# Optimization experiments

Measured on AMD Instinct MI355X. Metric: run time of the kernel, lower is better.

Reference implementation:

```python
import math
import jax, jax.numpy as jnp
import numpy as np

Q_MAX = 127.0  # 2**(8-1) - 1 for n_bits=8
SCALE_EPS = 1e-5


def _hadamard_matrix(n):
    H = np.array([[1.0]], dtype=np.float32)
    while H.shape[0] < n:
        H = np.block([[H, H], [H, -H]])
    return jnp.asarray(H)


def quantize_per_channel_absmax(w):
    # per output-channel absmax quantize-dequantize (torch weight per_channel)
    scales = jnp.clip(jnp.max(jnp.abs(w), axis=-1, keepdims=True) / Q_MAX, SCALE_EPS, None)
    return jnp.round(w / scales) * scales


def quantize_per_token_absmax(x):
    # per-token (last-dim) absmax quantize-dequantize
    scales = jnp.clip(jnp.max(jnp.abs(x), axis=-1, keepdims=True) / Q_MAX, SCALE_EPS, None)
    return jnp.round(x / scales) * scales


def setup_inputs() -> dict:
    key = jax.random.key(0)
    k1, k2, k3 = jax.random.split(key, 3)
    B, S, D_IN, D_OUT = 2, 2048, 4096, 4096
    x = jax.random.normal(k1, (B, S, D_IN), dtype=jnp.float32)
    # weight quantized at __init__ time (per_channel, 8-bit), as in the wrapper
    weight = quantize_per_channel_absmax(
        jax.random.normal(k2, (D_OUT, D_IN), dtype=jnp.float32) * (1.0 / math.sqrt(D_IN)))
    bias = jax.random.normal(k3, (D_OUT,), dtype=jnp.float32)
    return {"x": x, "weight": weight, "bias": bias, "had_dim": 64}


def reference(x, weight, bias, had_dim):
    # --- online_partial_had, K == 1 path ---
    B, S, D = x.shape
    n_groups = D // had_dim
    H = _hadamard_matrix(n_groups).astype(x.dtype)
    xr = x.reshape(-1, n_groups, had_dim)  # (B*S, G, had_dim)
    # hadamard_transform along the group axis, scale = 1/sqrt(G)
    xr = jnp.einsum('hg,bgd->bhd', H, xr) * (1.0 / math.sqrt(n_groups))
    x = xr.reshape(B, S, D)
    # --- per-token absmax activation quant ---
    x = quantize_per_token_absmax(x)
    # --- linear with (already quantized) weight ---
    return jnp.einsum('bsd,od->bso', x, weight) + bias
```

## Files before the change

### kernel.cpp

```cpp
#include <hip/hip_runtime.h>

#define M_DIM 4096
#define N_DIM 4096
#define K_DIM 4096

typedef __attribute__((ext_vector_type(4))) int i32x4;
typedef __attribute__((ext_vector_type(16))) int i32x16;

typedef __attribute__((address_space(1))) const void GV;
typedef __attribute__((address_space(3))) void LV;

__global__ __launch_bounds__(256) void prequant_kernel(const float* __restrict__ x,
                                                       const float* __restrict__ w,
                                                       char* __restrict__ xq,
                                                       char* __restrict__ wq,
                                                       float* __restrict__ sx,
                                                       float* __restrict__ sw) {
  const int wave = threadIdx.x >> 6;
  const int lane = threadIdx.x & 63;

  if (blockIdx.x >= 1024) {
    const int row = (blockIdx.x - 1024) * 4 + wave;
    const float* wp = w + (size_t)row * 4096;
    float4 v[16];
#pragma unroll
    for (int c = 0; c < 16; ++c) v[c] = *(const float4*)(wp + c * 256 + lane * 4);
    float amax = 0.f;
#pragma unroll
    for (int c = 0; c < 16; ++c)
      amax = fmaxf(amax, fmaxf(fmaxf(fabsf(v[c].x), fabsf(v[c].y)),
                               fmaxf(fabsf(v[c].z), fabsf(v[c].w))));
#pragma unroll
    for (int off = 32; off >= 1; off >>= 1) amax = fmaxf(amax, __shfl_xor(amax, off, 64));
    amax = fmaxf(amax, 1e-30f);
    const float inv = 127.0f / amax;
    char* op = wq + (size_t)row * 4096;
#pragma unroll
    for (int c = 0; c < 16; ++c) {
      char4 o;
      o.x = (char)rintf(v[c].x * inv);
      o.y = (char)rintf(v[c].y * inv);
      o.z = (char)rintf(v[c].z * inv);
      o.w = (char)rintf(v[c].w * inv);
      *(char4*)(op + c * 256 + lane * 4) = o;
    }
    if (lane == 0) sw[row] = amax * (1.0f / 127.0f);
    return;
  }

  const int tok = blockIdx.x * 4 + wave;
  const int gs = lane >> 4;
  const int q = lane & 15;
  const float* xp = x + (size_t)tok * 4096;

  float4 v[16];
#pragma unroll
  for (int gl = 0; gl < 16; ++gl)
    v[gl] = *(const float4*)(xp + (gl * 4 + gs) * 64 + q * 4);

#pragma unroll
  for (int s = 1; s < 16; s <<= 1) {
#pragma unroll
    for (int i = 0; i < 16; ++i) {
      if ((i & s) == 0) {
        float4 a = v[i], b = v[i | s];
        v[i].x = a.x + b.x; v[i].y = a.y + b.y; v[i].z = a.z + b.z; v[i].w = a.w + b.w;
        v[i | s].x = a.x - b.x; v[i | s].y = a.y - b.y;
        v[i | s].z = a.z - b.z; v[i | s].w = a.w - b.w;
      }
    }
  }
#pragma unroll
  for (int st = 0; st < 2; ++st) {
    const int L = 16 << st;
    const bool hi = (lane & L) != 0;
#pragma unroll
    for (int i = 0; i < 16; ++i) {
      float4 t;
      t.x = __shfl_xor(v[i].x, L, 64);
      t.y = __shfl_xor(v[i].y, L, 64);
      t.z = __shfl_xor(v[i].z, L, 64);
      t.w = __shfl_xor(v[i].w, L, 64);
      if (hi) {
        v[i].x = t.x - v[i].x; v[i].y = t.y - v[i].y;
        v[i].z = t.z - v[i].z; v[i].w = t.w - v[i].w;
      } else {
        v[i].x += t.x; v[i].y += t.y; v[i].z += t.z; v[i].w += t.w;
      }
    }
  }

  float amax = 0.f;
#pragma unroll
  for (int i = 0; i < 16; ++i) {
    v[i].x *= 0.125f; v[i].y *= 0.125f; v[i].z *= 0.125f; v[i].w *= 0.125f;
    amax = fmaxf(amax, fmaxf(fmaxf(fabsf(v[i].x), fabsf(v[i].y)),
                             fmaxf(fabsf(v[i].z), fabsf(v[i].w))));
  }
#pragma unroll
  for (int off = 32; off >= 1; off >>= 1) amax = fmaxf(amax, __shfl_xor(amax, off, 64));

  const float s = fmaxf(amax * (1.0f / 127.0f), 1e-5f);
  const float inv = 1.0f / s;

  char* op = xq + (size_t)tok * 4096;
#pragma unroll
  for (int gl = 0; gl < 16; ++gl) {
    char4 o;
    o.x = (char)rintf(v[gl].x * inv);
    o.y = (char)rintf(v[gl].y * inv);
    o.z = (char)rintf(v[gl].z * inv);
    o.w = (char)rintf(v[gl].w * inv);
    *(char4*)(op + (gl * 4 + gs) * 64 + q * 4) = o;
  }
  if (lane == 0) sx[tok] = s;
}

__global__ __launch_bounds__(256, 2) void gemm_i8(const char* __restrict__ A,
                                                  const char* __restrict__ B,
                                                  const float* __restrict__ sx,
                                                  const float* __restrict__ sw,
                                                  const float* __restrict__ bias,
                                                  float* __restrict__ C) {
  __shared__ __align__(16) char sm[73728];

  const int tid = threadIdx.x;
  const int lane = tid & 63;
  const int wave = tid >> 6;
  const int wm = wave >> 1;
  const int wn = wave & 1;
  const int m32 = lane & 31;
  const int half = lane >> 5;

  const int bid = blockIdx.x;
  const int cx = bid & 7, idx = bid >> 3;
  const int bm = (cx & 3) * 4 + (idx >> 4);
  const int bn = (cx >> 2) * 16 + (idx & 15);

  const int strow = tid >> 2;
  const int sseg = ((tid & 3) ^ ((tid >> 3) & 3)) << 4;
  const char* gA0 = A + (size_t)(bm * 256 + strow) * K_DIM + sseg;
  const char* gB0 = B + (size_t)(bn * 128 + strow) * K_DIM + sseg;

#define STAGE(BUFOFF, KO)                                                                \
  {                                                                                      \
    char* d_ = sm + (BUFOFF) + (tid << 4);                                               \
    __builtin_amdgcn_global_load_lds((GV*)(gA0 + (KO)), (LV*)d_, 16, 0, 0);              \
    __builtin_amdgcn_global_load_lds((GV*)(gA0 + 64 * (size_t)K_DIM + (KO)),             \
                                     (LV*)(d_ + 4096), 16, 0, 0);                        \
    __builtin_amdgcn_global_load_lds((GV*)(gA0 + 128 * (size_t)K_DIM + (KO)),            \
                                     (LV*)(d_ + 8192), 16, 0, 0);                        \
    __builtin_amdgcn_global_load_lds((GV*)(gA0 + 192 * (size_t)K_DIM + (KO)),            \
                                     (LV*)(d_ + 12288), 16, 0, 0);                       \
    __builtin_amdgcn_global_load_lds((GV*)(gB0 + (KO)), (LV*)(d_ + 16384), 16, 0, 0);    \
    __builtin_amdgcn_global_load_lds((GV*)(gB0 + 64 * (size_t)K_DIM + (KO)),             \
                                     (LV*)(d_ + 20480), 16, 0, 0);                       \
  }

  const int aBase = (wm * 128 + m32) * 64;
  const int bBase = 16384 + (wn * 64 + m32) * 64;
  int sl[2];
#pragma unroll
  for (int kc = 0; kc < 2; ++kc) sl[kc] = ((kc * 2 + half) ^ ((m32 >> 1) & 3)) << 4;

  i32x16 acc[4][2];
#pragma unroll
  for (int i = 0; i < 4; ++i)
#pragma unroll
    for (int j = 0; j < 2; ++j)
#pragma unroll
      for (int r = 0; r < 16; ++r) acc[i][j][r] = 0;

  STAGE(0, 0);
  STAGE(24576, 64);
  asm volatile("s_waitcnt vmcnt(6)" ::: "memory");
  __builtin_amdgcn_s_barrier();
  __builtin_amdgcn_sched_barrier(0);

  int o0 = 0, o1 = 24576, o2 = 49152;

#pragma unroll 1
  for (int t = 0; t < 64; ++t) {
    const char* bufp = sm + o0;

    i32x4 af[2][4], bf[2][2];
#pragma unroll
    for (int kc = 0; kc < 2; ++kc) {
#pragma unroll
      for (int fm = 0; fm < 4; ++fm)
        af[kc][fm] = *(const i32x4*)(bufp + aBase + fm * 2048 + sl[kc]);
#pragma unroll
      for (int fn = 0; fn < 2; ++fn)
        bf[kc][fn] = *(const i32x4*)(bufp + bBase + fn * 2048 + sl[kc]);
    }

    if (t < 62) STAGE(o2, (size_t)(t + 2) * 64);

    __builtin_amdgcn_s_setprio(1);
#pragma unroll
    for (int kc = 0; kc < 2; ++kc)
#pragma unroll
      for (int fm = 0; fm < 4; ++fm)
#pragma unroll
        for (int fn = 0; fn < 2; ++fn)
          acc[fm][fn] =
              __builtin_amdgcn_mfma_i32_32x32x32_i8(af[kc][fm], bf[kc][fn], acc[fm][fn], 0, 0, 0);
    __builtin_amdgcn_s_setprio(0);

    if (t < 62) {
      asm volatile("s_waitcnt vmcnt(6)" ::: "memory");
    } else if (t == 62) {
      asm volatile("s_waitcnt vmcnt(0)" ::: "memory");
    }
    if (t < 63) {
      __builtin_amdgcn_s_barrier();
      __builtin_amdgcn_sched_barrier(0);
    }
    const int tmp = o0; o0 = o1; o1 = o2; o2 = tmp;
  }
#undef STAGE

  const int col0 = bn * 128 + wn * 64 + m32;
  const float swv0 = sw[col0];
  const float swv1 = sw[col0 + 32];
  const float bv0 = bias[col0];
  const float bv1 = bias[col0 + 32];

#pragma unroll
  for (int fm = 0; fm < 4; ++fm) {
    const int rbase = bm * 256 + wm * 128 + fm * 32 + 4 * half;
    float sxv[16];
#pragma unroll
    for (int r = 0; r < 16; ++r) sxv[r] = sx[rbase + (r & 3) + 8 * (r >> 2)];
#pragma unroll
    for (int fn = 0; fn < 2; ++fn) {
      const int colg = col0 + fn * 32;
      const float swb = fn ? swv1 : swv0;
      const float bvb = fn ? bv1 : bv0;
#pragma unroll
      for (int r = 0; r < 16; ++r) {
        const int rowg = rbase + (r & 3) + 8 * (r >> 2);
        C[(size_t)rowg * N_DIM + colg] = (float)acc[fm][fn][r] * (sxv[r] * swb) + bvb;
      }
    }
  }
}

extern "C" void kernel_launch(void* const* d_in, const int* in_sizes, int n_in,
                              void* d_out, int out_size, void* d_ws, size_t ws_size,
                              hipStream_t stream) {
  const float* x = (const float*)d_in[0];
  const float* w = (const float*)d_in[1];
  const float* bias = (const float*)d_in[2];

  char* xq = (char*)d_ws;
  char* wq = xq + (size_t)M_DIM * K_DIM;
  float* sx = (float*)(wq + (size_t)N_DIM * K_DIM);
  float* sw = sx + M_DIM;
  float* out = (float*)d_out;

  prequant_kernel<<<2048, 256, 0, stream>>>(x, w, xq, wq, sx, sw);

  gemm_i8<<<dim3(512), dim3(256), 0, stream>>>(xq, wq, sx, sw, bias, out);
}
```

Baseline: 247.7 us.

## Prepack quantized weights in MFMA fragment order and load B directly to registers

The weight prequant pass now writes int8 weights in a pre-swizzled layout matching the MFMA B-fragment order, staging through LDS for coalesced stores. The GEMM no longer stages B tiles in shared memory. Each wave loads its B fragments straight from global memory into registers, double-buffered across even and odd k-steps, and LDS shrinks from 72KB to 48KB. This cuts LDS traffic and B ds_reads, but adds global-load latency exposure and more register pressure.

```diff
diff --git a/kernel.cpp b/kernel.cpp
--- a/kernel.cpp
+++ b/kernel.cpp
@@ -16,6 +16,7 @@
                                                        char* __restrict__ wq,
                                                        float* __restrict__ sx,
                                                        float* __restrict__ sw) {
+  __shared__ char lb[4][4096];
   const int wave = threadIdx.x >> 6;
   const int lane = threadIdx.x & 63;
 
@@ -34,7 +35,6 @@
     for (int off = 32; off >= 1; off >>= 1) amax = fmaxf(amax, __shfl_xor(amax, off, 64));
     amax = fmaxf(amax, 1e-30f);
     const float inv = 127.0f / amax;
-    char* op = wq + (size_t)row * 4096;
 #pragma unroll
     for (int c = 0; c < 16; ++c) {
       char4 o;
@@ -42,7 +42,14 @@
       o.y = (char)rintf(v[c].y * inv);
       o.z = (char)rintf(v[c].z * inv);
       o.w = (char)rintf(v[c].w * inv);
-      *(char4*)(op + c * 256 + lane * 4) = o;
+      *(char4*)(&lb[wave][c * 256 + lane * 4]) = o;
+    }
+    asm volatile("s_waitcnt lgkmcnt(0)" ::: "memory");
+    const size_t pbase = (size_t)(row >> 5) * 131072 + (size_t)(row & 31) * 16;
+#pragma unroll
+    for (int j = 0; j < 4; ++j) {
+      i32x4 ch = *(const i32x4*)(&lb[wave][lane * 64 + j * 16]);
+      *(i32x4*)(wq + pbase + (size_t)(2 * lane + (j >> 1)) * 1024 + (j & 1) * 512) = ch;
     }
     if (lane == 0) sw[row] = amax * (1.0f / 127.0f);
     return;
@@ -122,7 +129,7 @@
                                                   const float* __restrict__ sw,
                                                   const float* __restrict__ bias,
                                                   float* __restrict__ C) {
-  __shared__ __align__(16) char sm[73728];
+  __shared__ __align__(16) char sm[49152];
 
   const int tid = threadIdx.x;
   const int lane = tid & 63;
@@ -140,25 +147,25 @@
   const int strow = tid >> 2;
   const int sseg = ((tid & 3) ^ ((tid >> 3) & 3)) << 4;
   const char* gA0 = A + (size_t)(bm * 256 + strow) * K_DIM + sseg;
-  const char* gB0 = B + (size_t)(bn * 128 + strow) * K_DIM + sseg;
-
-#define STAGE(BUFOFF, KO)                                                                \
-  {                                                                                      \
-    char* d_ = sm + (BUFOFF) + (tid << 4);                                               \
-    __builtin_amdgcn_global_load_lds((GV*)(gA0 + (KO)), (LV*)d_, 16, 0, 0);              \
-    __builtin_amdgcn_global_load_lds((GV*)(gA0 + 64 * (size_t)K_DIM + (KO)),             \
-                                     (LV*)(d_ + 4096), 16, 0, 0);                        \
-    __builtin_amdgcn_global_load_lds((GV*)(gA0 + 128 * (size_t)K_DIM + (KO)),            \
-                                     (LV*)(d_ + 8192), 16, 0, 0);                        \
-    __builtin_amdgcn_global_load_lds((GV*)(gA0 + 192 * (size_t)K_DIM + (KO)),            \
-                                     (LV*)(d_ + 12288), 16, 0, 0);                       \
-    __builtin_amdgcn_global_load_lds((GV*)(gB0 + (KO)), (LV*)(d_ + 16384), 16, 0, 0);    \
-    __builtin_amdgcn_global_load_lds((GV*)(gB0 + 64 * (size_t)K_DIM + (KO)),             \
-                                     (LV*)(d_ + 20480), 16, 0, 0);                       \
-  }
+
+#define STAGE(BUFOFF, KO)                                                              \
+  {                                                                                    \
+    char* d_ = sm + (BUFOFF) + (tid << 4);                                             \
+    __builtin_amdgcn_global_load_lds((GV*)(gA0 + (KO)), (LV*)d_, 16, 0, 0);            \
+    __builtin_amdgcn_global_load_lds((GV*)(gA0 + 64 * (size_t)K_DIM + (KO)),           \
+                                     (LV*)(d_ + 4096), 16, 0, 0);                      \
+    __builtin_amdgcn_global_load_lds((GV*)(gA0 + 128 * (size_t)K_DIM + (KO)),          \
+                                     (LV*)(d_ + 8192), 16, 0, 0);                      \
+    __builtin_amdgcn_global_load_lds((GV*)(gA0 + 192 * (size_t)K_DIM + (KO)),          \
+                                     (LV*)(d_ + 12288), 16, 0, 0);                     \
+  }
+
+  const char* gBf[2];
+#pragma unroll
+  for (int fn = 0; fn < 2; ++fn)
+    gBf[fn] = B + (size_t)(bn * 4 + wn * 2 + fn) * 131072 + (lane << 4);
 
   const int aBase = (wm * 128 + m32) * 64;
-  const int bBase = 16384 + (wn * 64 + m32) * 64;
   int sl[2];
 #pragma unroll
   for (int kc = 0; kc < 2; ++kc) sl[kc] = ((kc * 2 + half) ^ ((m32 >> 1) & 3)) << 4;
@@ -171,53 +178,62 @@
 #pragma unroll
       for (int r = 0; r < 16; ++r) acc[i][j][r] = 0;
 
+  i32x4 bE[2][2], bO[2][2];
+
   STAGE(0, 0);
-  STAGE(24576, 64);
-  asm volatile("s_waitcnt vmcnt(6)" ::: "memory");
+#pragma unroll
+  for (int kc = 0; kc < 2; ++kc)
+#pragma unroll
+    for (int fn = 0; fn < 2; ++fn)
+      bE[kc][fn] = *(const i32x4*)(gBf[fn] + (size_t)kc * 1024);
+  STAGE(16384, 64);
+#pragma unroll
+  for (int kc = 0; kc < 2; ++kc)
+#pragma unroll
+    for (int fn = 0; fn < 2; ++fn)
+      bO[kc][fn] = *(const i32x4*)(gBf[fn] + (size_t)(2 + kc) * 1024);
+  asm volatile("s_waitcnt vmcnt(8)" ::: "memory");
   __builtin_amdgcn_s_barrier();
   __builtin_amdgcn_sched_barrier(0);
 
-  int o0 = 0, o1 = 24576, o2 = 49152;
+  int o0 = 0, o1 = 16384, o2 = 32768;
+
+#define TILE(T, BSET, DOPF, WAITSTR)                                                   \
+  {                                                                                    \
+    const char* bufp = sm + o0;                                                        \
+    i32x4 af[2][4];                                                                    \
+    _Pragma("unroll") for (int kc = 0; kc < 2; ++kc)                                   \
+      _Pragma("unroll") for (int fm = 0; fm < 4; ++fm)                                 \
+        af[kc][fm] = *(const i32x4*)(bufp + aBase + fm * 2048 + sl[kc]);               \
+    if (DOPF) STAGE(o2, (size_t)((T) + 2) * 64);                                       \
+    asm volatile("s_waitcnt lgkmcnt(0)" ::: "memory");                                 \
+    __builtin_amdgcn_sched_barrier(0);                                                 \
+    __builtin_amdgcn_s_setprio(1);                                                     \
+    _Pragma("unroll") for (int kc = 0; kc < 2; ++kc)                                   \
+      _Pragma("unroll") for (int fm = 0; fm < 4; ++fm)                                 \
+        _Pragma("unroll") for (int fn = 0; fn < 2; ++fn)                               \
+          acc[fm][fn] = __builtin_amdgcn_mfma_i32_32x32x32_i8(af[kc][fm], BSET[kc][fn], \
+                                                              acc[fm][fn], 0, 0, 0);   \
+    __builtin_amdgcn_s_setprio(0);                                                     \
+    if (DOPF) {                                                                        \
+      _Pragma("unroll") for (int kc = 0; kc < 2; ++kc)                                 \
+        _Pragma("unroll") for (int fn = 0; fn < 2; ++fn)                               \
+          BSET[kc][fn] = *(const i32x4*)(gBf[fn] + (size_t)(((T) + 2) * 2 + kc) * 1024); \
+    }                                                                                  \
+    asm volatile("s_waitcnt " WAITSTR ::: "memory");                                   \
+    __builtin_amdgcn_s_barrier();                                                      \
+    __builtin_amdgcn_sched_barrier(0);                                                 \
+    { const int tmp_ = o0; o0 = o1; o1 = o2; o2 = tmp_; }                              \
+  }
 
 #pragma unroll 1
-  for (int t = 0; t < 64; ++t) {
-    const char* bufp = sm + o0;
-
-    i32x4 af[2][4], bf[2][2];
-#pragma unroll
-    for (int kc = 0; kc < 2; ++kc) {
-#pragma unroll
-      for (int fm = 0; fm < 4; ++fm)
-        af[kc][fm] = *(const i32x4*)(bufp + aBase + fm * 2048 + sl[kc]);
-#pragma unroll
-      for (int fn = 0; fn < 2; ++fn)
-        bf[kc][fn] = *(const i32x4*)(bufp + bBase + fn * 2048 + sl[kc]);
-    }
-
-    if (t < 62) STAGE(o2, (size_t)(t + 2) * 64);
-
-    __builtin_amdgcn_s_setprio(1);
-#pragma unroll
-    for (int kc = 0; kc < 2; ++kc)
-#pragma unroll
-      for (int fm = 0; fm < 4; ++fm)
-#pragma unroll
-        for (int fn = 0; fn < 2; ++fn)
-          acc[fm][fn] =
-              __builtin_amdgcn_mfma_i32_32x32x32_i8(af[kc][fm], bf[kc][fn], acc[fm][fn], 0, 0, 0);
-    __builtin_amdgcn_s_setprio(0);
-
-    if (t < 62) {
-      asm volatile("s_waitcnt vmcnt(6)" ::: "memory");
-    } else if (t == 62) {
-      asm volatile("s_waitcnt vmcnt(0)" ::: "memory");
-    }
-    if (t < 63) {
-      __builtin_amdgcn_s_barrier();
-      __builtin_amdgcn_sched_barrier(0);
-    }
-    const int tmp = o0; o0 = o1; o1 = o2; o2 = tmp;
-  }
+  for (int p = 0; p < 31; ++p) {
+    TILE(2 * p, bE, 1, "vmcnt(8)");
+    TILE(2 * p + 1, bO, 1, "vmcnt(8)");
+  }
+  TILE(62, bE, 0, "vmcnt(0)");
+  TILE(63, bO, 0, "vmcnt(0)");
+#undef TILE
 #undef STAGE
 
   const int col0 = bn * 128 + wn * 64 + m32;
```

New measurement: 252.4 us. No clear change (+1.9%).
